# Kernel optimization log

Hardware: AMD Instinct MI355X
Metric: run time of the kernel (lower is better)

## Reference

```python
import jax, jax.numpy as jnp
import numpy as np

B, S, H, V = 4, 2048, 768, 32000
HID = 100          # self.hidden_size
N_LABELS = 3
LN2 = 0.6931471805599453


def setup_inputs() -> dict:
    key = jax.random.key(0)
    ks = jax.random.split(key, 10)
    return {
        "input_ids": jax.random.randint(ks[0], (B, S), 0, V),
        "attention_mask": jnp.ones((B, S), jnp.float32),
        "sentiment": jax.random.normal(ks[1], (B, 3), jnp.float32),
        "hidden_states": jax.random.normal(ks[2], (B, S, H), jnp.float32),
        "lm_logits": jax.random.normal(ks[3], (B, S, V), jnp.float32),
        "W_ih": jax.random.normal(ks[4], (4 * HID, H + 1), jnp.float32) * 0.05,
        "W_hh": jax.random.normal(ks[5], (4 * HID, HID), jnp.float32) * 0.05,
        "b_ih": jax.random.normal(ks[6], (4 * HID,), jnp.float32) * 0.05,
        "b_hh": jax.random.normal(ks[7], (4 * HID,), jnp.float32) * 0.05,
        "cls_W": jax.random.normal(ks[8], (N_LABELS, HID + 3), jnp.float32) * 0.05,
        "cls_b": jax.random.normal(ks[9], (N_LABELS,), jnp.float32) * 0.05,
    }


def _lstm_last(x, W_ih, W_hh, b_ih, b_hh):
    # x: [B,S,D] -> last hidden state [B,HID]; PyTorch gate order i,f,g,o
    b, hid = x.shape[0], W_hh.shape[1]
    x_proj = jnp.einsum('bsd,gd->bsg', x, W_ih) + b_ih + b_hh  # [B,S,4H]

    def step(carry, xt):
        h, c = carry
        gates = xt + h @ W_hh.T
        i, f, g, o = jnp.split(gates, 4, axis=-1)
        c = jax.nn.sigmoid(f) * c + jax.nn.sigmoid(i) * jnp.tanh(g)
        h = jax.nn.sigmoid(o) * jnp.tanh(c)
        return (h, c), None

    h0 = jnp.zeros((b, hid), x.dtype)
    (hT, _), _ = jax.lax.scan(step, (h0, h0), jnp.swapaxes(x_proj, 0, 1))
    return hT


def reference(input_ids, attention_mask, sentiment, hidden_states, lm_logits,
              W_ih, W_hh, b_ih, b_hh, cls_W, cls_b):
    # surprisal: -log2(softmax(logits)[input_ids]) * mask, detached
    log_p = jax.nn.log_softmax(lm_logits, axis=-1)                       # [B,S,V]
    lp = jnp.take_along_axis(log_p, input_ids[..., None], axis=2)[..., 0]  # [B,S]
    surp = jax.lax.stop_gradient((-lp / LN2) * attention_mask)

    x = jnp.concatenate([hidden_states, surp[..., None]], axis=-1)  # [B,S,H+1]
    hT = _lstm_last(x, W_ih, W_hh, b_ih, b_hh)                      # [B,HID]
    # dropout is identity at inference
    feat = jnp.concatenate([hT, sentiment], axis=1)                 # [B,HID+3]
    return feat @ cls_W.T + cls_b                                   # [B,N_LABELS]
```

## Files before the change

kernel.cpp:

```cpp
#include <hip/hip_runtime.h>
#include <hip/hip_bf16.h>
#include <math.h>

#define B 4
#define S 2048
#define H 768
#define V 32000
#define HID 100
#define G4 400
#define M_TOT (B*S)
#define PD 2

typedef _Float16 half2_t __attribute__((ext_vector_type(2)));
typedef _Float16 half8_t __attribute__((ext_vector_type(8)));

__device__ __forceinline__ float fdot2_(half2_t a, half2_t b, float c) {
#if __has_builtin(__builtin_amdgcn_fdot2)
  return __builtin_amdgcn_fdot2(a, b, c, false);
#else
  return c + (float)a[0] * (float)b[0] + (float)a[1] * (float)b[1];
#endif
}

__device__ __forceinline__ float sigmoidf_(float x) {
  return 1.0f / (1.0f + __expf(-x));
}

__device__ __forceinline__ void lds_barrier_() {
  asm volatile("s_waitcnt lgkmcnt(0)" ::: "memory");
  __builtin_amdgcn_s_barrier();
  asm volatile("" ::: "memory");
}

#define BM 64
#define BN 64
#define BK 32
#define NTM (M_TOT / BM)
#define NTN ((G4 + BN - 1) / BN)
#define NGEMM (NTM * NTN)
#define GRP 71

__global__ __launch_bounds__(256) void fused_pre_kernel(
    const float* __restrict__ logits, const int* __restrict__ ids,
    const float* __restrict__ mask, float* __restrict__ surp,
    const float* __restrict__ A,
    const float* __restrict__ W,
    const float* __restrict__ b_ih, const float* __restrict__ b_hh,
    float* __restrict__ xproj) {
  __shared__ float smem[BK * BM + BK * BN];
  int tid = threadIdx.x;
  int grp = blockIdx.x / GRP;
  int sub = blockIdx.x % GRP;

  if (sub < NTN) {
    float (*As)[BM] = (float(*)[BM])smem;
    float (*Bs)[BN] = (float(*)[BN])(smem + BK * BM);
    int m0 = grp * BM;
    int n0 = sub * BN;
    int tx = tid & 15, ty = tid >> 4;
    float acc[4][4] = {};
    for (int k0 = 0; k0 < H; k0 += BK) {
      #pragma unroll
      for (int l = 0; l < 2; ++l) {
        int idx = tid + l * 256;
        int row = idx >> 3;
        int kq = idx & 7;
        float4 v = *(const float4*)&A[(size_t)(m0 + row) * H + k0 + kq * 4];
        As[kq * 4 + 0][row] = v.x;
        As[kq * 4 + 1][row] = v.y;
        As[kq * 4 + 2][row] = v.z;
        As[kq * 4 + 3][row] = v.w;
      }
      #pragma unroll
      for (int l = 0; l < 8; ++l) {
        int idx = tid + l * 256;
        int n = idx >> 5;
        int kk = idx & 31;
        int gn = n0 + n;
        Bs[kk][n] = (gn < G4) ? W[(size_t)gn * (H + 1) + k0 + kk] : 0.0f;
      }
      __syncthreads();
      #pragma unroll
      for (int k = 0; k < BK; ++k) {
        float4 a = *(const float4*)&As[k][ty * 4];
        float4 bq = *(const float4*)&Bs[k][tx * 4];
        float av[4] = {a.x, a.y, a.z, a.w};
        float bv[4] = {bq.x, bq.y, bq.z, bq.w};
        #pragma unroll
        for (int i = 0; i < 4; ++i)
          #pragma unroll
          for (int j = 0; j < 4; ++j)
            acc[i][j] += av[i] * bv[j];
      }
      __syncthreads();
    }
    #pragma unroll
    for (int i = 0; i < 4; ++i) {
      int gm = m0 + ty * 4 + i;
      #pragma unroll
      for (int j = 0; j < 4; ++j) {
        int gn = n0 + tx * 4 + j;
        if (gn < G4) {
          float val = acc[i][j] + b_ih[gn] + b_hh[gn];
          int g = gn / HID, k = gn % HID;
          int pn = 4 * k + (((g & 1) << 1) | (g >> 1));
          xproj[(size_t)gm * G4 + pn] = val;
        }
      }
    }
  } else {
    int row = grp * 64 + (sub - NTN);
    const float* x = logits + (size_t)row * V;
    float m = -INFINITY, s = 0.0f;
    const float4* x4 = (const float4*)x;
    for (int i = tid; i < V / 4; i += 256) {
      float4 v = x4[i];
      float mv = fmaxf(fmaxf(v.x, v.y), fmaxf(v.z, v.w));
      if (mv > m) { s *= __expf(m - mv); m = mv; }
      s += __expf(v.x - m) + __expf(v.y - m) + __expf(v.z - m) + __expf(v.w - m);
    }
    #pragma unroll
    for (int off = 32; off > 0; off >>= 1) {
      float mo = __shfl_xor(m, off);
      float so = __shfl_xor(s, off);
      float mn = fmaxf(m, mo);
      s = s * __expf(m - mn) + so * __expf(mo - mn);
      m = mn;
    }
    float* sm = smem;
    float* ss = smem + 4;
    int wid = tid >> 6, lane = tid & 63;
    if (lane == 0) { sm[wid] = m; ss[wid] = s; }
    __syncthreads();
    if (tid == 0) {
      float M = sm[0], Ssum = ss[0];
      #pragma unroll
      for (int w = 1; w < 4; ++w) {
        float mo = sm[w], so = ss[w];
        float mn = fmaxf(M, mo);
        Ssum = Ssum * __expf(M - mn) + so * __expf(mo - mn);
        M = mn;
      }
      float xid = x[ids[row]];
      surp[row] = (M + __logf(Ssum) - xid) * 1.4426950408889634f * mask[row];
    }
  }
}

#define NH2 52
__global__ __launch_bounds__(256, 1) void lstm_kernel(
    const float* __restrict__ xproj,
    const float* __restrict__ surp,
    const float* __restrict__ W_ih,
    const float* __restrict__ W_hh,
    const float* __restrict__ sent,
    const float* __restrict__ cls_W,
    const float* __restrict__ cls_b,
    float* __restrict__ out) {
  int b = blockIdx.x;
  int tid = threadIdx.x;
  __shared__ __align__(16) _Float16 hb0[2 * NH2];
  __shared__ __align__(16) _Float16 hb1[2 * NH2];

  bool active = tid < 200;
  int q = active ? tid : 199;
  int k = q >> 1;
  bool odd = (q & 1) != 0;
  int rA = odd ? (HID + k) : k;
  int rB = odd ? (3 * HID + k) : (2 * HID + k);

  half2_t wA[NH2], wB[NH2];
  float wlA, wlB;
  {
    const float* pA = W_hh + (size_t)rA * HID;
    const float* pB = W_hh + (size_t)rB * HID;
    #pragma unroll
    for (int j = 0; j < 50; ++j) {
      wA[j] = half2_t{(_Float16)pA[2 * j], (_Float16)pA[2 * j + 1]};
      wB[j] = half2_t{(_Float16)pB[2 * j], (_Float16)pB[2 * j + 1]};
    }
    #pragma unroll
    for (int j = 50; j < NH2; ++j) { wA[j] = half2_t{0, 0}; wB[j] = half2_t{0, 0}; }
    wlA = W_ih[(size_t)rA * (H + 1) + H];
    wlB = W_ih[(size_t)rB * (H + 1) + H];
  }

  float c_reg = 0.0f;
  if (tid < 2 * NH2) { hb0[tid] = (_Float16)0; hb1[tid] = (_Float16)0; }
  __syncthreads();

  const float* xp = xproj + (size_t)b * S * G4;
  const float* sp = surp + (size_t)b * S;
  float2 xr[PD];
  float sr[PD];
  #pragma unroll
  for (int d = 0; d < PD; ++d) {
    xr[d] = ((const float2*)(xp + (size_t)d * G4))[q];
    sr[d] = sp[d];
  }

  #pragma unroll 2
  for (int t = 0; t < S; ++t) {
    int slot = t & (PD - 1);
    const half8_t* hr = (t & 1) ? (const half8_t*)hb0 : (const half8_t*)hb1;
    _Float16* hw = (t & 1) ? hb1 : hb0;

    float2 xv = xr[slot];
    float sv = sr[slot];
    {
      int tp = (t + PD < S) ? (t + PD) : (S - 1);
      xr[slot] = ((const float2*)(xp + (size_t)tp * G4))[q];
      sr[slot] = sp[tp];
    }

    float a0 = 0.f, a1 = 0.f, b0 = 0.f, b1 = 0.f;
    #pragma unroll
    for (int j = 0; j < 13; ++j) {
      half8_t hv = hr[j];
      half2_t h0 = {hv[0], hv[1]}, h1 = {hv[2], hv[3]};
      half2_t h2 = {hv[4], hv[5]}, h3 = {hv[6], hv[7]};
      a0 = fdot2_(wA[4 * j + 0], h0, a0);
      b0 = fdot2_(wB[4 * j + 0], h0, b0);
      a1 = fdot2_(wA[4 * j + 1], h1, a1);
      b1 = fdot2_(wB[4 * j + 1], h1, b1);
      a0 = fdot2_(wA[4 * j + 2], h2, a0);
      b0 = fdot2_(wB[4 * j + 2], h2, b0);
      a1 = fdot2_(wA[4 * j + 3], h3, a1);
      b1 = fdot2_(wB[4 * j + 3], h3, b1);
    }
    float aA = a0 + a1 + xv.x + sv * wlA;
    float aB = b0 + b1 + xv.y + sv * wlB;

    float vA = sigmoidf_(aA);
    float sB = sigmoidf_(odd ? aB : 2.0f * aB);
    float vB = odd ? sB : (2.0f * sB - 1.0f);

    float f_n = __shfl_xor(vA, 1);
    float o_n = __shfl_xor(vB, 1);

    c_reg = f_n * c_reg + vA * vB;
    float tc = 2.0f * sigmoidf_(2.0f * c_reg) - 1.0f;
    float h = o_n * tc;
    if (active && !odd) hw[k] = (_Float16)h;

    lds_barrier_();
  }

  if (tid < 3) {
    float acc = cls_b[tid];
    const float* cw = cls_W + tid * (HID + 3);
    #pragma unroll
    for (int j = 0; j < HID; ++j) acc += cw[j] * (float)hb1[j];
    #pragma unroll
    for (int k2 = 0; k2 < 3; ++k2) acc += cw[HID + k2] * sent[b * 3 + k2];
    out[b * 3 + tid] = acc;
  }
}

extern "C" void kernel_launch(void* const* d_in, const int* in_sizes, int n_in,
                              void* d_out, int out_size, void* d_ws, size_t ws_size,
                              hipStream_t stream) {
  const int*   input_ids = (const int*)d_in[0];
  const float* mask      = (const float*)d_in[1];
  const float* sent      = (const float*)d_in[2];
  const float* hs        = (const float*)d_in[3];
  const float* logits    = (const float*)d_in[4];
  const float* W_ih      = (const float*)d_in[5];
  const float* W_hh      = (const float*)d_in[6];
  const float* b_ih      = (const float*)d_in[7];
  const float* b_hh      = (const float*)d_in[8];
  const float* cls_W     = (const float*)d_in[9];
  const float* cls_b     = (const float*)d_in[10];
  float* out = (float*)d_out;

  float* surp  = (float*)d_ws;
  float* xproj = surp + M_TOT;

  fused_pre_kernel<<<GRP * 128, 256, 0, stream>>>(
      logits, input_ids, mask, surp, hs, W_ih, b_ih, b_hh, xproj);
  lstm_kernel<<<B, 256, 0, stream>>>(xproj, surp, W_ih, W_hh, sent, cls_W,
                                     cls_b, out);
}
```

Before: 1.506 ms.

## Merge pre-pass and LSTM into one kernel with per-tile readiness counters

Fuses the logsumexp/GEMM pre-kernel and the LSTM recurrence into a single launch. LSTM blocks take the lowest block IDs and spin on per-64-row atomic counters, so the serial recurrence can start as soon as its input tiles are ready instead of after the whole pre-pass. Surprisal rows are reordered to interleave batches, the logits loads become nontemporal, and surprisal values are loaded four at a time. The scheme adds a memset and spin-wait overhead, and it assumes the LSTM blocks are co-resident with the producer blocks, otherwise it can deadlock.

```diff
diff --git a/kernel.cpp b/kernel.cpp
--- a/kernel.cpp
+++ b/kernel.cpp
@@ -11,8 +11,22 @@
 #define M_TOT (B*S)
 #define PD 2
 
+#define BM 64
+#define BN 64
+#define BK 32
+#define NTM (M_TOT / BM)
+#define NTN ((G4 + BN - 1) / BN)
+#define NGEMM (NTM * NTN)
+#define NLSTM B
+#define GEMM_BASE NLSTM
+#define SURP_BASE (NLSTM + NGEMM)
+#define NBLK (SURP_BASE + M_TOT)
+#define TARGET (NTN + BM)
+#define NH2 52
+
 typedef _Float16 half2_t __attribute__((ext_vector_type(2)));
 typedef _Float16 half8_t __attribute__((ext_vector_type(8)));
+typedef float f4v __attribute__((ext_vector_type(4)));
 
 __device__ __forceinline__ float fdot2_(half2_t a, half2_t b, float c) {
 #if __has_builtin(__builtin_amdgcn_fdot2)
@@ -32,31 +46,72 @@
   asm volatile("" ::: "memory");
 }
 
-#define BM 64
-#define BN 64
-#define BK 32
-#define NTM (M_TOT / BM)
-#define NTN ((G4 + BN - 1) / BN)
-#define NGEMM (NTM * NTN)
-#define GRP 71
-
-__global__ __launch_bounds__(256) void fused_pre_kernel(
+__device__ __forceinline__ void wait_tile_(int* cnt, int idx) {
+  while (__hip_atomic_load(&cnt[idx], __ATOMIC_ACQUIRE,
+                           __HIP_MEMORY_SCOPE_AGENT) < TARGET)
+    __builtin_amdgcn_s_sleep(2);
+}
+
+__global__ __launch_bounds__(256, 1) void mega_kernel(
     const float* __restrict__ logits, const int* __restrict__ ids,
-    const float* __restrict__ mask, float* __restrict__ surp,
-    const float* __restrict__ A,
-    const float* __restrict__ W,
+    const float* __restrict__ mask,
+    const float* __restrict__ hs,
+    const float* __restrict__ W_ih,
+    const float* __restrict__ W_hh,
     const float* __restrict__ b_ih, const float* __restrict__ b_hh,
-    float* __restrict__ xproj) {
-  __shared__ float smem[BK * BM + BK * BN];
+    const float* __restrict__ sent, const float* __restrict__ cls_W,
+    const float* __restrict__ cls_b,
+    float* __restrict__ surp, float* __restrict__ xproj,
+    int* cnt, float* __restrict__ out) {
+  __shared__ __align__(16) float smem[BK * BM + BK * BN];
   int tid = threadIdx.x;
-  int grp = blockIdx.x / GRP;
-  int sub = blockIdx.x % GRP;
-
-  if (sub < NTN) {
+  int bid = blockIdx.x;
+
+  if (bid >= SURP_BASE) {
+    int j = bid - SURP_BASE;
+    int row = (j & 3) * S + (j >> 2);
+    const float* x = logits + (size_t)row * V;
+    float m = -INFINITY, s = 0.0f;
+    const f4v* x4 = (const f4v*)x;
+    for (int i = tid; i < V / 4; i += 256) {
+      f4v v = __builtin_nontemporal_load(x4 + i);
+      float mv = fmaxf(fmaxf(v[0], v[1]), fmaxf(v[2], v[3]));
+      if (mv > m) { s *= __expf(m - mv); m = mv; }
+      s += __expf(v[0] - m) + __expf(v[1] - m) + __expf(v[2] - m) + __expf(v[3] - m);
+    }
+    #pragma unroll
+    for (int off = 32; off > 0; off >>= 1) {
+      float mo = __shfl_xor(m, off);
+      float so = __shfl_xor(s, off);
+      float mn = fmaxf(m, mo);
+      s = s * __expf(m - mn) + so * __expf(mo - mn);
+      m = mn;
+    }
+    float* sm = smem;
+    float* ss = smem + 4;
+    int wid = tid >> 6, lane = tid & 63;
+    if (lane == 0) { sm[wid] = m; ss[wid] = s; }
+    __syncthreads();
+    if (tid == 0) {
+      float M = sm[0], Ssum = ss[0];
+      #pragma unroll
+      for (int w = 1; w < 4; ++w) {
+        float mo = sm[w], so = ss[w];
+        float mn = fmaxf(M, mo);
+        Ssum = Ssum * __expf(M - mn) + so * __expf(mo - mn);
+        M = mn;
+      }
+      float xid = x[ids[row]];
+      surp[row] = (M + __logf(Ssum) - xid) * 1.4426950408889634f * mask[row];
+      __hip_atomic_fetch_add(&cnt[row >> 6], 1, __ATOMIC_RELEASE,
+                             __HIP_MEMORY_SCOPE_AGENT);
+    }
+  } else if (bid >= GEMM_BASE) {
     float (*As)[BM] = (float(*)[BM])smem;
     float (*Bs)[BN] = (float(*)[BN])(smem + BK * BM);
-    int m0 = grp * BM;
-    int n0 = sub * BN;
+    int g = bid - GEMM_BASE;
+    int m0 = (g / NTN) * BM;
+    int n0 = (g % NTN) * BN;
     int tx = tid & 15, ty = tid >> 4;
     float acc[4][4] = {};
     for (int k0 = 0; k0 < H; k0 += BK) {
@@ -65,7 +120,7 @@
         int idx = tid + l * 256;
         int row = idx >> 3;
         int kq = idx & 7;
-        float4 v = *(const float4*)&A[(size_t)(m0 + row) * H + k0 + kq * 4];
+        float4 v = *(const float4*)&hs[(size_t)(m0 + row) * H + k0 + kq * 4];
         As[kq * 4 + 0][row] = v.x;
         As[kq * 4 + 1][row] = v.y;
         As[kq * 4 + 2][row] = v.z;
@@ -77,7 +132,7 @@
         int n = idx >> 5;
         int kk = idx & 31;
         int gn = n0 + n;
-        Bs[kk][n] = (gn < G4) ? W[(size_t)gn * (H + 1) + k0 + kk] : 0.0f;
+        Bs[kk][n] = (gn < G4) ? W_ih[(size_t)gn * (H + 1) + k0 + kk] : 0.0f;
       }
       __syncthreads();
       #pragma unroll
@@ -102,158 +157,128 @@
         int gn = n0 + tx * 4 + j;
         if (gn < G4) {
           float val = acc[i][j] + b_ih[gn] + b_hh[gn];
-          int g = gn / HID, k = gn % HID;
-          int pn = 4 * k + (((g & 1) << 1) | (g >> 1));
+          int gg = gn / HID, kk = gn % HID;
+          int pn = 4 * kk + (((gg & 1) << 1) | (gg >> 1));
           xproj[(size_t)gm * G4 + pn] = val;
         }
       }
     }
+    __syncthreads();
+    if (tid == 0)
+      __hip_atomic_fetch_add(&cnt[m0 >> 6], 1, __ATOMIC_RELEASE,
+                             __HIP_MEMORY_SCOPE_AGENT);
   } else {
-    int row = grp * 64 + (sub - NTN);
-    const float* x = logits + (size_t)row * V;
-    float m = -INFINITY, s = 0.0f;
-    const float4* x4 = (const float4*)x;
-    for (int i = tid; i < V / 4; i += 256) {
-      float4 v = x4[i];
-      float mv = fmaxf(fmaxf(v.x, v.y), fmaxf(v.z, v.w));
-      if (mv > m) { s *= __expf(m - mv); m = mv; }
-      s += __expf(v.x - m) + __expf(v.y - m) + __expf(v.z - m) + __expf(v.w - m);
-    }
+    int b = bid;
+    _Float16* hb0 = (_Float16*)smem;
+    _Float16* hb1 = ((_Float16*)smem) + 128;
+
+    bool active = tid < 200;
+    int q = active ? tid : 199;
+    int k = q >> 1;
+    bool odd = (q & 1) != 0;
+    int rA = odd ? (HID + k) : k;
+    int rB = odd ? (3 * HID + k) : (2 * HID + k);
+
+    half2_t wA[NH2], wB[NH2];
+    float wlA, wlB;
+    {
+      const float* pA = W_hh + (size_t)rA * HID;
+      const float* pB = W_hh + (size_t)rB * HID;
+      #pragma unroll
+      for (int j = 0; j < 50; ++j) {
+        wA[j] = half2_t{(_Float16)pA[2 * j], (_Float16)pA[2 * j + 1]};
+        wB[j] = half2_t{(_Float16)pB[2 * j], (_Float16)pB[2 * j + 1]};
+      }
+      #pragma unroll
+      for (int j = 50; j < NH2; ++j) { wA[j] = half2_t{0, 0}; wB[j] = half2_t{0, 0}; }
+      wlA = W_ih[(size_t)rA * (H + 1) + H];
+      wlB = W_ih[(size_t)rB * (H + 1) + H];
+    }
+
+    float c_reg = 0.0f;
+    if (tid < 104) { hb0[tid] = (_Float16)0; hb1[tid] = (_Float16)0; }
+    __syncthreads();
+
+    const float* xp = xproj + (size_t)b * S * G4;
+    const float* sp = surp + (size_t)b * S;
+    int tile0 = b * 32;
+
+    wait_tile_(cnt, tile0);
+
+    float2 xr[PD];
     #pragma unroll
-    for (int off = 32; off > 0; off >>= 1) {
-      float mo = __shfl_xor(m, off);
-      float so = __shfl_xor(s, off);
-      float mn = fmaxf(m, mo);
-      s = s * __expf(m - mn) + so * __expf(mo - mn);
-      m = mn;
-    }
-    float* sm = smem;
-    float* ss = smem + 4;
-    int wid = tid >> 6, lane = tid & 63;
-    if (lane == 0) { sm[wid] = m; ss[wid] = s; }
-    __syncthreads();
-    if (tid == 0) {
-      float M = sm[0], Ssum = ss[0];
-      #pragma unroll
-      for (int w = 1; w < 4; ++w) {
-        float mo = sm[w], so = ss[w];
-        float mn = fmaxf(M, mo);
-        Ssum = Ssum * __expf(M - mn) + so * __expf(mo - mn);
-        M = mn;
-      }
-      float xid = x[ids[row]];
-      surp[row] = (M + __logf(Ssum) - xid) * 1.4426950408889634f * mask[row];
-    }
-  }
-}
-
-#define NH2 52
-__global__ __launch_bounds__(256, 1) void lstm_kernel(
-    const float* __restrict__ xproj,
-    const float* __restrict__ surp,
-    const float* __restrict__ W_ih,
-    const float* __restrict__ W_hh,
-    const float* __restrict__ sent,
-    const float* __restrict__ cls_W,
-    const float* __restrict__ cls_b,
-    float* __restrict__ out) {
-  int b = blockIdx.x;
-  int tid = threadIdx.x;
-  __shared__ __align__(16) _Float16 hb0[2 * NH2];
-  __shared__ __align__(16) _Float16 hb1[2 * NH2];
-
-  bool active = tid < 200;
-  int q = active ? tid : 199;
-  int k = q >> 1;
-  bool odd = (q & 1) != 0;
-  int rA = odd ? (HID + k) : k;
-  int rB = odd ? (3 * HID + k) : (2 * HID + k);
-
-  half2_t wA[NH2], wB[NH2];
-  float wlA, wlB;
-  {
-    const float* pA = W_hh + (size_t)rA * HID;
-    const float* pB = W_hh + (size_t)rB * HID;
-    #pragma unroll
-    for (int j = 0; j < 50; ++j) {
-      wA[j] = half2_t{(_Float16)pA[2 * j], (_Float16)pA[2 * j + 1]};
-      wB[j] = half2_t{(_Float16)pB[2 * j], (_Float16)pB[2 * j + 1]};
-    }
-    #pragma unroll
-    for (int j = 50; j < NH2; ++j) { wA[j] = half2_t{0, 0}; wB[j] = half2_t{0, 0}; }
-    wlA = W_ih[(size_t)rA * (H + 1) + H];
-    wlB = W_ih[(size_t)rB * (H + 1) + H];
-  }
-
-  float c_reg = 0.0f;
-  if (tid < 2 * NH2) { hb0[tid] = (_Float16)0; hb1[tid] = (_Float16)0; }
-  __syncthreads();
-
-  const float* xp = xproj + (size_t)b * S * G4;
-  const float* sp = surp + (size_t)b * S;
-  float2 xr[PD];
-  float sr[PD];
-  #pragma unroll
-  for (int d = 0; d < PD; ++d) {
-    xr[d] = ((const float2*)(xp + (size_t)d * G4))[q];
-    sr[d] = sp[d];
-  }
-
-  #pragma unroll 2
-  for (int t = 0; t < S; ++t) {
-    int slot = t & (PD - 1);
-    const half8_t* hr = (t & 1) ? (const half8_t*)hb0 : (const half8_t*)hb1;
-    _Float16* hw = (t & 1) ? hb1 : hb0;
-
-    float2 xv = xr[slot];
-    float sv = sr[slot];
-    {
-      int tp = (t + PD < S) ? (t + PD) : (S - 1);
-      xr[slot] = ((const float2*)(xp + (size_t)tp * G4))[q];
-      sr[slot] = sp[tp];
-    }
-
-    float a0 = 0.f, a1 = 0.f, b0 = 0.f, b1 = 0.f;
-    #pragma unroll
-    for (int j = 0; j < 13; ++j) {
-      half8_t hv = hr[j];
-      half2_t h0 = {hv[0], hv[1]}, h1 = {hv[2], hv[3]};
-      half2_t h2 = {hv[4], hv[5]}, h3 = {hv[6], hv[7]};
-      a0 = fdot2_(wA[4 * j + 0], h0, a0);
-      b0 = fdot2_(wB[4 * j + 0], h0, b0);
-      a1 = fdot2_(wA[4 * j + 1], h1, a1);
-      b1 = fdot2_(wB[4 * j + 1], h1, b1);
-      a0 = fdot2_(wA[4 * j + 2], h2, a0);
-      b0 = fdot2_(wB[4 * j + 2], h2, b0);
-      a1 = fdot2_(wA[4 * j + 3], h3, a1);
-      b1 = fdot2_(wB[4 * j + 3], h3, b1);
-    }
-    float aA = a0 + a1 + xv.x + sv * wlA;
-    float aB = b0 + b1 + xv.y + sv * wlB;
-
-    float vA = sigmoidf_(aA);
-    float sB = sigmoidf_(odd ? aB : 2.0f * aB);
-    float vB = odd ? sB : (2.0f * sB - 1.0f);
-
-    float f_n = __shfl_xor(vA, 1);
-    float o_n = __shfl_xor(vB, 1);
-
-    c_reg = f_n * c_reg + vA * vB;
-    float tc = 2.0f * sigmoidf_(2.0f * c_reg) - 1.0f;
-    float h = o_n * tc;
-    if (active && !odd) hw[k] = (_Float16)h;
-
-    lds_barrier_();
-  }
-
-  if (tid < 3) {
-    float acc = cls_b[tid];
-    const float* cw = cls_W + tid * (HID + 3);
-    #pragma unroll
-    for (int j = 0; j < HID; ++j) acc += cw[j] * (float)hb1[j];
-    #pragma unroll
-    for (int k2 = 0; k2 < 3; ++k2) acc += cw[HID + k2] * sent[b * 3 + k2];
-    out[b * 3 + tid] = acc;
+    for (int d = 0; d < PD; ++d)
+      xr[d] = ((const float2*)(xp + (size_t)d * G4))[q];
+    float4 sv_cur = *(const float4*)sp;
+    float4 sv_nxt = sv_cur;
+
+    #pragma unroll 4
+    for (int t = 0; t < S; ++t) {
+      if ((t & 63) == 0) {
+        int nc = (t >> 6) + 1;
+        if (nc > 31) nc = 31;
+        wait_tile_(cnt, tile0 + nc);
+      }
+      int slot = t & (PD - 1);
+      const half8_t* hr = (t & 1) ? (const half8_t*)hb0 : (const half8_t*)hb1;
+      _Float16* hw = (t & 1) ? hb1 : hb0;
+
+      float2 xv = xr[slot];
+      int ph = t & 3;
+      float sv = ph == 0 ? sv_cur.x : ph == 1 ? sv_cur.y
+               : ph == 2 ? sv_cur.z : sv_cur.w;
+      if (ph == 0) {
+        int tp = t + 4; if (tp > S - 4) tp = S - 4;
+        sv_nxt = *(const float4*)(sp + tp);
+      }
+      {
+        int tp = (t + PD < S) ? (t + PD) : (S - 1);
+        xr[slot] = ((const float2*)(xp + (size_t)tp * G4))[q];
+      }
+
+      float a0 = 0.f, a1 = 0.f, b0 = 0.f, b1 = 0.f;
+      #pragma unroll
+      for (int j = 0; j < 13; ++j) {
+        half8_t hv = hr[j];
+        half2_t h0 = {hv[0], hv[1]}, h1 = {hv[2], hv[3]};
+        half2_t h2 = {hv[4], hv[5]}, h3 = {hv[6], hv[7]};
+        a0 = fdot2_(wA[4 * j + 0], h0, a0);
+        b0 = fdot2_(wB[4 * j + 0], h0, b0);
+        a1 = fdot2_(wA[4 * j + 1], h1, a1);
+        b1 = fdot2_(wB[4 * j + 1], h1, b1);
+        a0 = fdot2_(wA[4 * j + 2], h2, a0);
+        b0 = fdot2_(wB[4 * j + 2], h2, b0);
+        a1 = fdot2_(wA[4 * j + 3], h3, a1);
+        b1 = fdot2_(wB[4 * j + 3], h3, b1);
+      }
+      float aA = a0 + a1 + xv.x + sv * wlA;
+      float aB = b0 + b1 + xv.y + sv * wlB;
+
+      float vA = sigmoidf_(aA);
+      float sB = sigmoidf_(odd ? aB : 2.0f * aB);
+      float vB = odd ? sB : (2.0f * sB - 1.0f);
+
+      float f_n = __shfl_xor(vA, 1);
+      float o_n = __shfl_xor(vB, 1);
+
+      c_reg = f_n * c_reg + vA * vB;
+      float tc = 2.0f * sigmoidf_(2.0f * c_reg) - 1.0f;
+      float h = o_n * tc;
+      if (active && !odd) hw[k] = (_Float16)h;
+
+      if (ph == 3) sv_cur = sv_nxt;
+      lds_barrier_();
+    }
+
+    if (tid < 3) {
+      float acc = cls_b[tid];
+      const float* cw = cls_W + tid * (HID + 3);
+      #pragma unroll
+      for (int j = 0; j < HID; ++j) acc += cw[j] * (float)hb1[j];
+      #pragma unroll
+      for (int k2 = 0; k2 < 3; ++k2) acc += cw[HID + k2] * sent[b * 3 + k2];
+      out[b * 3 + tid] = acc;
+    }
   }
 }
 
@@ -275,9 +300,10 @@
 
   float* surp  = (float*)d_ws;
   float* xproj = surp + M_TOT;
-
-  fused_pre_kernel<<<GRP * 128, 256, 0, stream>>>(
-      logits, input_ids, mask, surp, hs, W_ih, b_ih, b_hh, xproj);
-  lstm_kernel<<<B, 256, 0, stream>>>(xproj, surp, W_ih, W_hh, sent, cls_W,
-                                     cls_b, out);
-}
+  int*   cnt   = (int*)(xproj + (size_t)M_TOT * G4);
+
+  hipMemsetAsync(cnt, 0, NTM * sizeof(int), stream);
+  mega_kernel<<<NBLK, 256, 0, stream>>>(
+      logits, input_ids, mask, hs, W_ih, W_hh, b_ih, b_hh,
+      sent, cls_W, cls_b, surp, xproj, cnt, out);
+}
```

Measured after the change: 1.506 ms. About the same (-0.0%).
